# Performance work log

Hardware: AMD Instinct MI355X
Metric: run time of the kernel (lower is better)

## Reference

```python
import jax, jax.numpy as jnp
import numpy as np

B, N, M, F, D, OUT = 2, 8192, 8192, 128, 3, 512

def setup_inputs() -> dict:
    key = jax.random.key(0)
    k1, k2, k3, k4, k5 = jax.random.split(key, 5)
    return {
        'geometry': jax.random.normal(k1, (B, N, D), dtype=jnp.float32),
        'gaussian_pcd': jax.random.normal(k2, (B, M, D), dtype=jnp.float32),
        'features': jax.random.normal(k3, (B, M, F), dtype=jnp.float32),
        'W_proj': jax.random.normal(k4, (OUT, F), dtype=jnp.float32) / np.sqrt(F),
        'b_proj': jax.random.normal(k5, (OUT,), dtype=jnp.float32) * 0.01,
        'k': 10,
    }

def reference(geometry, gaussian_pcd, features, W_proj, b_proj, k):
    # cdist via ||q||^2 + ||p||^2 - 2 q.p (matches torch.cdist matmul mode)
    q2 = jnp.sum(geometry * geometry, axis=-1)            # [B,N]
    p2 = jnp.sum(gaussian_pcd * gaussian_pcd, axis=-1)    # [B,M]
    d2 = q2[:, :, None] + p2[:, None, :] - 2.0 * jnp.einsum('bnd,bmd->bnm', geometry, gaussian_pcd)
    dists = jnp.sqrt(jnp.maximum(d2, 0.0))                # [B,N,M]
    # k smallest, sorted ascending
    neg_d, idx = jax.lax.top_k(-dists, k)                 # [B,N,k]
    knn_d = -neg_d
    # gather knn features: [B,N,k,F]
    knn_f = jax.vmap(lambda f, i: f[i])(features, idx)
    # inverse-distance weights, normalized
    w = 1.0 / (knn_d + 1e-8)
    w = w / jnp.sum(w, axis=-1, keepdims=True)
    interp = jnp.einsum('bnk,bnkf->bnf', w, knn_f)        # [B,N,F]
    # gaussian_feature_proj: Linear(128 -> feature_dim)
    return jnp.einsum('bnf,of->bno', interp, W_proj) + b_proj
```

## Files before the change

### kernel.cpp

```cpp
#include <hip/hip_runtime.h>
#include <math.h>

#define NQ    8192
#define NP    8192
#define NF    128
#define NOUT  512
#define NB    2
#define KNN   10
#define BNQ   (NB*NQ)
#define CELLS 4096

typedef unsigned long long u64;
typedef unsigned int u32;
typedef unsigned short ushort_t;
typedef __attribute__((ext_vector_type(8))) short bf16x8;
typedef __attribute__((ext_vector_type(4))) float f32x4;

__device__ const float EDGEX[17] = {
  -1e30f, -1.53412f, -1.15035f, -0.88715f, -0.67449f, -0.48878f, -0.31864f,
  -0.15731f, 0.0f, 0.15731f, 0.31864f, 0.48878f, 0.67449f, 0.88715f,
  1.15035f, 1.53412f, 1e30f };

__device__ __forceinline__ int bucket(float v) {
  int c = 0;
  c += (v > -1.53412f); c += (v > -1.15035f); c += (v > -0.88715f);
  c += (v > -0.67449f); c += (v > -0.48878f); c += (v > -0.31864f);
  c += (v > -0.15731f); c += (v > 0.0f);      c += (v > 0.15731f);
  c += (v > 0.31864f);  c += (v > 0.48878f);  c += (v > 0.67449f);
  c += (v > 0.88715f);  c += (v > 1.15035f);  c += (v > 1.53412f);
  return c;
}

__device__ __forceinline__ u64 shfl64(u64 v, int src) {
  unsigned lo = (unsigned)__shfl((int)(unsigned)(v & 0xffffffffull), src, 64);
  unsigned hi = (unsigned)__shfl((int)(unsigned)(v >> 32), src, 64);
  return ((u64)hi << 32) | lo;
}
__device__ __forceinline__ u64 shflup64(u64 v) {
  unsigned lo = (unsigned)__shfl_up((int)(unsigned)(v & 0xffffffffull), 1, 64);
  unsigned hi = (unsigned)__shfl_up((int)(unsigned)(v >> 32), 1, 64);
  return ((u64)hi << 32) | lo;
}

__device__ __forceinline__ unsigned fmono(float f) {
  unsigned u = __float_as_uint(f);
  return u ^ ((unsigned)((int)u >> 31) | 0x80000000u);
}
__device__ __forceinline__ float nextupf(float f) {
  unsigned u = __float_as_uint(f);
  unsigned n = (u & 0x80000000u) ? ((u == 0x80000000u) ? 1u : u - 1u) : u + 1u;
  return __uint_as_float(n);
}

__device__ __forceinline__ float wmin64f(float v) {
#pragma unroll
  for (int off = 1; off < 64; off <<= 1)
    v = fminf(v, __shfl_xor(v, off, 64));
  return v;
}

__device__ __forceinline__ void insert_loop(float d2, int idxv, int lane,
                                            u64& lst, float& dlv, float& th) {
  for (;;) {
    u64 mask = __ballot(d2 < th);
    if (!mask) break;
    int src = __builtin_ctzll(mask);
    float cd = __uint_as_float(
        (unsigned)__builtin_amdgcn_readlane(__float_as_int(d2), src));
    int  ci = __builtin_amdgcn_readlane(idxv, src);
    u64 kk = ((u64)fmono(cd) << 32) | (u32)ci;
    u64   prev  = shflup64(lst);
    float prevd = __shfl(dlv, lane - 1, 64);
    bool mylt = lst < kk;
    bool pins = (lane == 0) || (prev < kk);
    lst = mylt ? lst : (pins ? kk : prev);
    dlv = mylt ? dlv : (pins ? cd : prevd);
    float d9 = __uint_as_float(
        (unsigned)__builtin_amdgcn_readlane(__float_as_int(dlv), 9));
    th = fminf(th, nextupf(d9));
    if (lane == src) d2 = __builtin_nanf("");
  }
}

__device__ __forceinline__ ushort_t f2bf(float x) {
  unsigned u = __float_as_uint(x);
  return (ushort_t)((u + 0x7FFFu + ((u >> 16) & 1u)) >> 16);
}

__global__ __launch_bounds__(256) void prep_kernel(
    const float* __restrict__ W, ushort_t* __restrict__ Wb,
    int* __restrict__ hist)
{
  const int tid = blockIdx.x * 256 + threadIdx.x;
  Wb[tid] = f2bf(W[tid]);
  if (tid < NB * CELLS) hist[tid] = 0;
}

__global__ __launch_bounds__(256) void hist_kernel(
    const float* __restrict__ gpcd, int* __restrict__ hist)
{
  const int tid = blockIdx.x * 256 + threadIdx.x;
  const float* p = gpcd + (size_t)tid * 3;
  const int cell = (bucket(p[0]) << 8) | (bucket(p[1]) << 4) | bucket(p[2]);
  atomicAdd(&hist[(tid >> 13) * CELLS + cell], 1);
}

__global__ __launch_bounds__(1024) void scan_kernel(
    const int* __restrict__ hist, int* __restrict__ cellstart,
    int* __restrict__ cursor)
{
  __shared__ int tot[1024];
  const int t = threadIdx.x;
  int v[8]; int s = 0;
#pragma unroll
  for (int i = 0; i < 8; ++i) { v[i] = hist[t * 8 + i]; s += v[i]; }
  tot[t] = s;
  __syncthreads();
  int x = s;
  for (int off = 1; off < 1024; off <<= 1) {
    int y = 0;
    if (t >= off && ((t >= 512) == ((t - off) >= 512))) y = tot[t - off];
    __syncthreads();
    x += y; tot[t] = x;
    __syncthreads();
  }
  int run = x - s;
#pragma unroll
  for (int i = 0; i < 8; ++i) {
    const int cf = t * 8 + i;
    const int b = cf >> 12, c = cf & (CELLS - 1);
    cellstart[b * (CELLS + 1) + c] = run;
    cursor[cf] = run;
    run += v[i];
  }
  if (t == 0) {
    cellstart[CELLS] = NP;
    cellstart[(CELLS + 1) + CELLS] = NP;
  }
}

__global__ __launch_bounds__(256) void scatter_kernel(
    const float* __restrict__ gpcd, int* __restrict__ cursor,
    float4* __restrict__ sortedPts, int* __restrict__ sortedIdx)
{
  const int tid = blockIdx.x * 256 + threadIdx.x;
  const int b = tid >> 13, m = tid & 8191;
  const float* p = gpcd + (size_t)tid * 3;
  const float x = p[0], y = p[1], z = p[2];
  const int cell = (bucket(x) << 8) | (bucket(y) << 4) | bucket(z);
  const int pos = atomicAdd(&cursor[b * CELLS + cell], 1);
  sortedPts[(b << 13) + pos] = make_float4(x, y, z, x * x + y * y + z * z);
  sortedIdx[(b << 13) + pos] = m;
}

__global__ __launch_bounds__(256) void knn_interp_grid(
    const float* __restrict__ geometry,
    const float4* __restrict__ sortedPts, const int* __restrict__ sortedIdx,
    const int* __restrict__ cellstart, const float* __restrict__ features,
    ushort_t* __restrict__ Abf)
{
  const int lane = threadIdx.x & 63;
  const int q    = (blockIdx.x << 2) | (threadIdx.x >> 6);
  const int b    = q >> 13;

  const float* g = geometry + (size_t)q * 3;
  const float qx = g[0], qy = g[1], qz = g[2];
  const float q2 = qx * qx + qy * qy + qz * qz;
  const float c2x = -2.f * qx, c2y = -2.f * qy, c2z = -2.f * qz;
  const int cx = bucket(qx), cy = bucket(qy), cz = bucket(qz);

  const float4* __restrict__ SP = sortedPts + ((size_t)b << 13);
  const int*    __restrict__ SI = sortedIdx + ((size_t)b << 13);
  const int*    __restrict__ CS = cellstart + b * (CELLS + 1);

  u64   list = ~0ull;
  float dl   = INFINITY;
  float th   = INFINITY;
  bool  firstbatch = true;

  for (int s = 1; s <= 15; ++s) {
    const int w20 = 2 * s - 1;
    const u32 Mw  = (0x100000u + (u32)w20 - 1) / (u32)w20;
    const int Scap = 8 * s + 2 * w20 * w20;
    const int S = Scap + (s == 1 ? 1 : 0);
    for (int segbase = 0; segbase < S; segbase += 64) {
      const int k = segbase + lane;
      int st = 0, len = 0;
      if (k < S) {
        int x, y, zlo, zhi; bool valid;
        if (k < 8 * s) {
          const int twos = 2 * s;
          int side = 0, t = k;
          if (t >= twos) { ++side; t -= twos; }
          if (t >= twos) { ++side; t -= twos; }
          if (t >= twos) { ++side; t -= twos; }
          int dx, dy;
          if      (side == 0) { dx = -s + t; dy = -s; }
          else if (side == 1) { dx = s;      dy = -s + t; }
          else if (side == 2) { dx = s - t;  dy = s; }
          else                { dx = -s;     dy = s - t; }
          x = cx + dx; y = cy + dy;
          zlo = max(cz - s, 0); zhi = min(cz + s, 15);
          valid = (x >= 0) & (x < 16) & (y >= 0) & (y < 16);
        } else if (k < Scap) {
          const int kp = k - 8 * s;
          const u32 jj = (u32)(kp >> 1);
          const int z  = (kp & 1) ? (cz + s) : (cz - s);
          const u32 qd = (jj * Mw) >> 20;
          const u32 rm = jj - qd * (u32)w20;
          x = cx - (s - 1) + (int)rm;
          y = cy - (s - 1) + (int)qd;
          zlo = zhi = z;
          valid = (x >= 0) & (x < 16) & (y >= 0) & (y < 16) & (z >= 0) & (z < 16);
        } else {
          x = cx; y = cy; zlo = zhi = cz; valid = true;
        }
        if (valid) {
          const int base = ((x << 4) | y) << 4;
          st  = CS[base + zlo];
          len = CS[base + zhi + 1] - st;
        }
      }
      int pre = len;
#pragma unroll
      for (int off = 1; off < 64; off <<= 1) {
        int t2 = __shfl_up(pre, off, 64);
        if (lane >= off) pre += t2;
      }
      const int total = __shfl(pre, 63, 64);
      pre -= len;
      for (int cb = 0; cb < total; cb += 64) {
        const int j  = cb + lane;
        const int jc = min(j, total - 1);
        int r = 0;
#pragma unroll
        for (int off = 32; off; off >>= 1) {
          const int c = r + off;
          const int pc = __shfl(pre, c & 63, 64);
          if (c < 64 && pc <= jc) r = c;
        }
        const int o = __shfl(st, r, 64) + (jc - __shfl(pre, r, 64));
        const float4 p = SP[o];
        const int   idv = SI[o];
        float d2 = fmaf(c2x, p.x, fmaf(c2y, p.y, fmaf(c2z, p.z, q2 + p.w)));
        d2 = fmaxf(d2, 0.f);
        if (j >= total) d2 = __builtin_nanf("");

        if (firstbatch) {
          float lm = d2;
          float tau = INFINITY;
#pragma unroll
          for (int r2 = 0; r2 < KNN; ++r2) {
            tau = wmin64f(lm);
            u64 mk = __ballot(lm == tau);
            int w2 = __builtin_ctzll(mk);
            if (lane == w2) lm = INFINITY;
          }
          th = fminf(th, nextupf(tau));
          firstbatch = false;
        }
        insert_loop(d2, idv, lane, list, dl, th);
      }
    }
    const float d2_10 = __uint_as_float(
        (unsigned)__builtin_amdgcn_readlane(__float_as_int(dl), 9));
    float m = fminf(qx - EDGEX[max(cx - s, 0)], EDGEX[min(cx + s + 1, 16)] - qx);
    m = fminf(m, fminf(qy - EDGEX[max(cy - s, 0)], EDGEX[min(cy + s + 1, 16)] - qy));
    m = fminf(m, fminf(qz - EDGEX[max(cz - s, 0)], EDGEX[min(cz + s + 1, 16)] - qz));
    if (d2_10 <= m * m) break;
  }

  const float* __restrict__ F = features + (size_t)b * NP * NF;
  float w = 1.0f / (sqrtf(dl) + 1e-8f);
  float wsum = 0.0f;
#pragma unroll
  for (int jj = 0; jj < KNN; ++jj) wsum += __shfl(w, jj, 64);

  float a0 = 0.0f, a1 = 0.0f;
#pragma unroll
  for (int jj = 0; jj < KNN; ++jj) {
    float wj = __shfl(w, jj, 64) / wsum;
    int  mi  = (int)(u32)(shfl64(list, jj) & 0xffffffffull);
    const float2 f2 = *(const float2*)(F + (size_t)mi * NF + (lane << 1));
    a0 = fmaf(wj, f2.x, a0);
    a1 = fmaf(wj, f2.y, a1);
  }
  unsigned pack = (unsigned)f2bf(a0) | ((unsigned)f2bf(a1) << 16);
  *(unsigned*)(Abf + (size_t)q * NF + (lane << 1)) = pack;
}

__global__ __launch_bounds__(256) void proj_mfma(
    const ushort_t* __restrict__ Abf, const ushort_t* __restrict__ Wb,
    const float* __restrict__ bias, float* __restrict__ out)
{
  const int lane = threadIdx.x & 63;
  const int w    = threadIdx.x >> 6;
  const int mt   = blockIdx.x & 127;
  const int ot   = blockIdx.x >> 7;
  const int m0   = (mt << 7) + ((w & 1) << 6);
  const int o0   = (ot << 6) + ((w >> 1) << 5);
  const int r    = lane & 15;
  const int kg   = (lane >> 4) << 3;

  f32x4 acc[4][2];
#pragma unroll
  for (int i = 0; i < 4; ++i)
#pragma unroll
    for (int jn = 0; jn < 2; ++jn) acc[i][jn] = (f32x4)0.0f;

#pragma unroll
  for (int ks = 0; ks < 4; ++ks) {
    const int k0 = (ks << 5) + kg;
    bf16x8 a[4], bb[2];
#pragma unroll
    for (int i = 0; i < 4; ++i)
      a[i] = *(const bf16x8*)(Abf + (size_t)(m0 + (i << 4) + r) * NF + k0);
#pragma unroll
    for (int jn = 0; jn < 2; ++jn)
      bb[jn] = *(const bf16x8*)(Wb + (size_t)(o0 + (jn << 4) + r) * NF + k0);
#pragma unroll
    for (int i = 0; i < 4; ++i)
#pragma unroll
      for (int jn = 0; jn < 2; ++jn)
        acc[i][jn] = __builtin_amdgcn_mfma_f32_16x16x32_bf16(
            a[i], bb[jn], acc[i][jn], 0, 0, 0);
  }

  const int crow = (lane >> 4) << 2;
#pragma unroll
  for (int jn = 0; jn < 2; ++jn) {
    const int oc = o0 + (jn << 4) + r;
    const float bv = bias[oc];
#pragma unroll
    for (int i = 0; i < 4; ++i) {
#pragma unroll
      for (int reg = 0; reg < 4; ++reg) {
        const int qm = m0 + (i << 4) + crow + reg;
        out[(size_t)qm * NOUT + oc] = acc[i][jn][reg] + bv;
      }
    }
  }
}

extern "C" void kernel_launch(void* const* d_in, const int* in_sizes, int n_in,
                              void* d_out, int out_size, void* d_ws, size_t ws_size,
                              hipStream_t stream) {
  const float* geometry = (const float*)d_in[0];
  const float* gpcd     = (const float*)d_in[1];
  const float* features = (const float*)d_in[2];
  const float* W        = (const float*)d_in[3];
  const float* bias     = (const float*)d_in[4];
  float* out = (float*)d_out;

  char* ws = (char*)d_ws;
  size_t off = 0;
  ushort_t* Abf  = (ushort_t*)(ws + off); off += (size_t)BNQ * NF * 2;
  float4* sortedPts = (float4*)(ws + off); off += (size_t)NB * NP * 16;
  ushort_t* Wb   = (ushort_t*)(ws + off); off += (size_t)NOUT * NF * 2;
  int* hist      = (int*)(ws + off); off += (size_t)NB * CELLS * 4;
  int* cellstart = (int*)(ws + off); off += (size_t)NB * (CELLS + 1) * 4 + 8;
  int* cursor    = (int*)(ws + off); off += (size_t)NB * CELLS * 4;
  int* sortedIdx = (int*)(ws + off); off += (size_t)NB * NP * 4;

  prep_kernel<<<256, 256, 0, stream>>>(W, Wb, hist);
  hist_kernel<<<64, 256, 0, stream>>>(gpcd, hist);
  scan_kernel<<<1, 1024, 0, stream>>>(hist, cellstart, cursor);
  scatter_kernel<<<64, 256, 0, stream>>>(gpcd, cursor, sortedPts, sortedIdx);
  knn_interp_grid<<<BNQ / 4, 256, 0, stream>>>(geometry, sortedPts, sortedIdx,
                                               cellstart, features, Abf);
  proj_mfma<<<(BNQ / 128) * (NOUT / 64), 256, 0, stream>>>(Abf, Wb, bias, out);
}
```

Before: 130.9 us.

## Sort query points by grid cell before KNN search for locality

Query points are now bucketed into the same 16x16x16 grid as the reference points and scattered into cell-sorted order. The histogram, scan and scatter kernels are extended to handle both point sets. The KNN kernel processes queries in sorted order, so neighbouring wavefronts touch the same cells and candidate points, which should improve cache reuse and reduce divergence in search radius. Results are written back to each query's original row. The cost is extra atomics and a sortedQ buffer, and feature writes to Abf become scattered.

```diff
diff --git a/kernel.cpp b/kernel.cpp
--- a/kernel.cpp
+++ b/kernel.cpp
@@ -89,31 +89,42 @@
 
 __global__ __launch_bounds__(256) void prep_kernel(
     const float* __restrict__ W, ushort_t* __restrict__ Wb,
-    int* __restrict__ hist)
+    int* __restrict__ histall)
 {
   const int tid = blockIdx.x * 256 + threadIdx.x;
   Wb[tid] = f2bf(W[tid]);
-  if (tid < NB * CELLS) hist[tid] = 0;
-}
-
-__global__ __launch_bounds__(256) void hist_kernel(
-    const float* __restrict__ gpcd, int* __restrict__ hist)
+  if (tid < 2 * NB * CELLS) histall[tid] = 0;
+}
+
+__global__ __launch_bounds__(256) void hist2_kernel(
+    const float* __restrict__ gpcd, const float* __restrict__ geometry,
+    int* __restrict__ hist, int* __restrict__ qhist)
 {
   const int tid = blockIdx.x * 256 + threadIdx.x;
-  const float* p = gpcd + (size_t)tid * 3;
-  const int cell = (bucket(p[0]) << 8) | (bucket(p[1]) << 4) | bucket(p[2]);
-  atomicAdd(&hist[(tid >> 13) * CELLS + cell], 1);
-}
-
-__global__ __launch_bounds__(1024) void scan_kernel(
-    const int* __restrict__ hist, int* __restrict__ cellstart,
-    int* __restrict__ cursor)
+  if (tid < NB * NP) {
+    const float* p = gpcd + (size_t)tid * 3;
+    const int cell = (bucket(p[0]) << 8) | (bucket(p[1]) << 4) | bucket(p[2]);
+    atomicAdd(&hist[(tid >> 13) * CELLS + cell], 1);
+  } else {
+    const int qt = tid - NB * NP;
+    const float* g = geometry + (size_t)qt * 3;
+    const int cell = (bucket(g[0]) << 8) | (bucket(g[1]) << 4) | bucket(g[2]);
+    atomicAdd(&qhist[(qt >> 13) * CELLS + cell], 1);
+  }
+}
+
+__global__ __launch_bounds__(1024) void scan2_kernel(
+    const int* __restrict__ hist, const int* __restrict__ qhist,
+    int* __restrict__ cellstart, int* __restrict__ cursor,
+    int* __restrict__ qcursor)
 {
   __shared__ int tot[1024];
   const int t = threadIdx.x;
+  const bool isQ = blockIdx.x != 0;
+  const int* __restrict__ src = isQ ? qhist : hist;
   int v[8]; int s = 0;
 #pragma unroll
-  for (int i = 0; i < 8; ++i) { v[i] = hist[t * 8 + i]; s += v[i]; }
+  for (int i = 0; i < 8; ++i) { v[i] = src[t * 8 + i]; s += v[i]; }
   tot[t] = s;
   __syncthreads();
   int x = s;
@@ -129,42 +140,59 @@
   for (int i = 0; i < 8; ++i) {
     const int cf = t * 8 + i;
     const int b = cf >> 12, c = cf & (CELLS - 1);
-    cellstart[b * (CELLS + 1) + c] = run;
-    cursor[cf] = run;
+    if (isQ) {
+      qcursor[cf] = run;
+    } else {
+      cellstart[b * (CELLS + 1) + c] = run;
+      cursor[cf] = run;
+    }
     run += v[i];
   }
-  if (t == 0) {
+  if (!isQ && t == 0) {
     cellstart[CELLS] = NP;
     cellstart[(CELLS + 1) + CELLS] = NP;
   }
 }
 
-__global__ __launch_bounds__(256) void scatter_kernel(
-    const float* __restrict__ gpcd, int* __restrict__ cursor,
-    float4* __restrict__ sortedPts, int* __restrict__ sortedIdx)
+__global__ __launch_bounds__(256) void scatter2_kernel(
+    const float* __restrict__ gpcd, const float* __restrict__ geometry,
+    int* __restrict__ cursor, int* __restrict__ qcursor,
+    float4* __restrict__ sortedPts, int* __restrict__ sortedIdx,
+    float4* __restrict__ sortedQ)
 {
   const int tid = blockIdx.x * 256 + threadIdx.x;
-  const int b = tid >> 13, m = tid & 8191;
-  const float* p = gpcd + (size_t)tid * 3;
-  const float x = p[0], y = p[1], z = p[2];
-  const int cell = (bucket(x) << 8) | (bucket(y) << 4) | bucket(z);
-  const int pos = atomicAdd(&cursor[b * CELLS + cell], 1);
-  sortedPts[(b << 13) + pos] = make_float4(x, y, z, x * x + y * y + z * z);
-  sortedIdx[(b << 13) + pos] = m;
+  if (tid < NB * NP) {
+    const int b = tid >> 13, m = tid & 8191;
+    const float* p = gpcd + (size_t)tid * 3;
+    const float x = p[0], y = p[1], z = p[2];
+    const int cell = (bucket(x) << 8) | (bucket(y) << 4) | bucket(z);
+    const int pos = atomicAdd(&cursor[b * CELLS + cell], 1);
+    sortedPts[(b << 13) + pos] = make_float4(x, y, z, x * x + y * y + z * z);
+    sortedIdx[(b << 13) + pos] = m;
+  } else {
+    const int qt = tid - NB * NP;
+    const int b = qt >> 13, m = qt & 8191;
+    const float* g = geometry + (size_t)qt * 3;
+    const float x = g[0], y = g[1], z = g[2];
+    const int cell = (bucket(x) << 8) | (bucket(y) << 4) | bucket(z);
+    const int pos = atomicAdd(&qcursor[b * CELLS + cell], 1);
+    sortedQ[(b << 13) + pos] = make_float4(x, y, z, __int_as_float(m));
+  }
 }
 
 __global__ __launch_bounds__(256) void knn_interp_grid(
-    const float* __restrict__ geometry,
+    const float4* __restrict__ sortedQ,
     const float4* __restrict__ sortedPts, const int* __restrict__ sortedIdx,
     const int* __restrict__ cellstart, const float* __restrict__ features,
     ushort_t* __restrict__ Abf)
 {
   const int lane = threadIdx.x & 63;
-  const int q    = (blockIdx.x << 2) | (threadIdx.x >> 6);
-  const int b    = q >> 13;
-
-  const float* g = geometry + (size_t)q * 3;
-  const float qx = g[0], qy = g[1], qz = g[2];
+  const int qs   = (blockIdx.x << 2) | (threadIdx.x >> 6);
+  const int b    = qs >> 13;
+
+  const float4 sq = sortedQ[qs];
+  const float qx = sq.x, qy = sq.y, qz = sq.z;
+  const int morig = __float_as_int(sq.w);
   const float q2 = qx * qx + qy * qy + qz * qz;
   const float c2x = -2.f * qx, c2y = -2.f * qy, c2z = -2.f * qz;
   const int cx = bucket(qx), cy = bucket(qy), cz = bucket(qz);
@@ -286,7 +314,7 @@
     a1 = fmaf(wj, f2.y, a1);
   }
   unsigned pack = (unsigned)f2bf(a0) | ((unsigned)f2bf(a1) << 16);
-  *(unsigned*)(Abf + (size_t)q * NF + (lane << 1)) = pack;
+  *(unsigned*)(Abf + (size_t)((b << 13) + morig) * NF + (lane << 1)) = pack;
 }
 
 __global__ __launch_bounds__(256) void proj_mfma(
@@ -356,17 +384,22 @@
   size_t off = 0;
   ushort_t* Abf  = (ushort_t*)(ws + off); off += (size_t)BNQ * NF * 2;
   float4* sortedPts = (float4*)(ws + off); off += (size_t)NB * NP * 16;
+  float4* sortedQ   = (float4*)(ws + off); off += (size_t)BNQ * 16;
   ushort_t* Wb   = (ushort_t*)(ws + off); off += (size_t)NOUT * NF * 2;
-  int* hist      = (int*)(ws + off); off += (size_t)NB * CELLS * 4;
+  int* histall   = (int*)(ws + off); off += (size_t)2 * NB * CELLS * 4;
+  int* hist      = histall;
+  int* qhist     = histall + NB * CELLS;
   int* cellstart = (int*)(ws + off); off += (size_t)NB * (CELLS + 1) * 4 + 8;
   int* cursor    = (int*)(ws + off); off += (size_t)NB * CELLS * 4;
+  int* qcursor   = (int*)(ws + off); off += (size_t)NB * CELLS * 4;
   int* sortedIdx = (int*)(ws + off); off += (size_t)NB * NP * 4;
 
-  prep_kernel<<<256, 256, 0, stream>>>(W, Wb, hist);
-  hist_kernel<<<64, 256, 0, stream>>>(gpcd, hist);
-  scan_kernel<<<1, 1024, 0, stream>>>(hist, cellstart, cursor);
-  scatter_kernel<<<64, 256, 0, stream>>>(gpcd, cursor, sortedPts, sortedIdx);
-  knn_interp_grid<<<BNQ / 4, 256, 0, stream>>>(geometry, sortedPts, sortedIdx,
+  prep_kernel<<<256, 256, 0, stream>>>(W, Wb, histall);
+  hist2_kernel<<<128, 256, 0, stream>>>(gpcd, geometry, hist, qhist);
+  scan2_kernel<<<2, 1024, 0, stream>>>(hist, qhist, cellstart, cursor, qcursor);
+  scatter2_kernel<<<128, 256, 0, stream>>>(gpcd, geometry, cursor, qcursor,
+                                           sortedPts, sortedIdx, sortedQ);
+  knn_interp_grid<<<BNQ / 4, 256, 0, stream>>>(sortedQ, sortedPts, sortedIdx,
                                                cellstart, features, Abf);
   proj_mfma<<<(BNQ / 128) * (NOUT / 64), 256, 0, stream>>>(Abf, Wb, bias, out);
 }
```

Result: slower. 136.0 us (+3.9%).
